# Performance work log

Hardware: AMD Instinct MI355X
Metric: run time of the kernel (lower is better)

Reference implementation:

```python
import jax, jax.numpy as jnp
import numpy as np

T, N, C, D, S = 512, 32, 1296, 512, 30
NORM_SCALE = 32.0
NEGINF = -1e9


def setup_inputs() -> dict:
    key = jax.random.key(0)
    k1, k2, k3, k4, k5 = jax.random.split(key, 5)
    feats = jax.random.normal(k1, (T * N, D), dtype=jnp.float32)
    classifier_weight = jax.random.normal(k2, (D, C), dtype=jnp.float32)
    labeling = jax.random.randint(k3, (N, S), 1, C)  # targets cannot be blank(0)
    logit_lgts = (T - jax.random.randint(k4, (N,), 0, 32)).astype(jnp.int32)
    labeling_lgts = (S - jax.random.randint(k5, (N,), 0, 5)).astype(jnp.int32)
    return dict(feats=feats, classifier_weight=classifier_weight,
                labeling=labeling, logit_lgts=logit_lgts, labeling_lgts=labeling_lgts)


def _ctc_loss(log_probs, labels, in_lens, lab_lens):
    # log_probs: (T, N, C); labels: (N, S); blank = 0; reduction = 'sum'
    Tt, Nn, Cc = log_probs.shape
    Ss = labels.shape[1]
    L = 2 * Ss + 1
    # extended labeling: blank, l1, blank, l2, ..., blank  -> (N, L)
    ext = jnp.zeros((Nn, L), dtype=labels.dtype).at[:, 1::2].set(labels)
    # gather per-state log-probs: (T, N, L)
    lp_ext = jnp.take_along_axis(log_probs, jnp.broadcast_to(ext[None], (Tt, Nn, L)), axis=2)
    # skip transition s-2 -> s allowed iff s > 1 and ext[s] != ext[s-2]
    skip_ok = jnp.concatenate(
        [jnp.zeros((Nn, 2), dtype=bool), ext[:, 2:] != ext[:, :-2]], axis=1)
    alpha0 = (jnp.full((Nn, L), NEGINF, dtype=log_probs.dtype)
              .at[:, 0].set(lp_ext[0, :, 0])
              .at[:, 1].set(lp_ext[0, :, 1]))

    def step(alpha, inp):
        lp_t, t = inp  # lp_t: (N, L)
        a1 = alpha
        a2 = jnp.pad(alpha[:, :-1], ((0, 0), (1, 0)), constant_values=NEGINF)
        a3 = jnp.where(skip_ok,
                       jnp.pad(alpha[:, :-2], ((0, 0), (2, 0)), constant_values=NEGINF),
                       NEGINF)
        new = jax.nn.logsumexp(jnp.stack([a1, a2, a3], axis=0), axis=0) + lp_t
        # freeze alpha once t reaches a sample's input length
        alpha = jnp.where((t < in_lens)[:, None], new, alpha)
        return alpha, None

    alpha, _ = jax.lax.scan(step, alpha0, (lp_ext[1:], jnp.arange(1, Tt)))
    Ln = 2 * lab_lens + 1  # (N,)
    last = jnp.take_along_axis(alpha, (Ln - 1)[:, None], axis=1)[:, 0]
    last2 = jnp.take_along_axis(alpha, (Ln - 2)[:, None], axis=1)[:, 0]
    nll = -jnp.logaddexp(last, last2)
    return jnp.sum(nll)


def reference(feats, classifier_weight, labeling, logit_lgts, labeling_lgts):
    # RadialCTC: cosine logits with norm_scale, then CTC on log-softmax.
    w_n = classifier_weight / jnp.linalg.norm(classifier_weight, axis=0, keepdims=True)  # (D, C)
    f_n = feats / jnp.linalg.norm(feats, axis=1, keepdims=True)  # (T*N, D)
    logits = NORM_SCALE * (f_n @ w_n)  # (T*N, C)
    log_probs = jax.nn.log_softmax(logits.reshape(T, N, C), axis=-1)
    return _ctc_loss(log_probs, labeling, logit_lgts, labeling_lgts)
```

## Files before the change

kernel.cpp:

```cpp
#include <hip/hip_runtime.h>
#include <stdint.h>
#include <stddef.h>


typedef _Float16 f16;
typedef _Float16 f16x8 __attribute__((ext_vector_type(8)));
typedef float f32x4 __attribute__((ext_vector_type(4)));
typedef __attribute__((address_space(1))) void* as1_void_ptr;
typedef __attribute__((address_space(3))) void* as3_void_ptr;

#define TT 512
#define NN 32
#define CC 1296
#define DD 512
#define SS 30
#define CP 1408
#define LL 61
#define NEGINF (-1e9f)
#define NORM_SCALE 32.0f
#define LOG2E 1.4426950408889634f
#define LN2   0.6931471805599453f

__device__ __forceinline__ float fexp2(float x) { return __builtin_amdgcn_exp2f(x); }
__device__ __forceinline__ float flog2(float x) { return __builtin_amdgcn_logf(x); }

__device__ __forceinline__ double dpp_sr1_zero64(double x) {
    long long b = __double_as_longlong(x);
    int lo = (int)(b & 0xFFFFFFFFLL);
    int hi = (int)(b >> 32);
    int lo2 = __builtin_amdgcn_update_dpp(0, lo, 0x138, 0xF, 0xF, false);
    int hi2 = __builtin_amdgcn_update_dpp(0, hi, 0x138, 0xF, 0xF, false);
    return __longlong_as_double(((long long)hi2 << 32) |
                                (unsigned long long)(unsigned int)lo2);
}
template <int CTRL>
__device__ __forceinline__ int dpp_imax_level(int m) {
    int t = __builtin_amdgcn_update_dpp(0, m, CTRL, 0xF, 0xF, false);
    return m > t ? m : t;
}

__global__ void colnorm_kernel(const float* __restrict__ W, float* __restrict__ ssq) {
    int c = blockIdx.x * 64 + threadIdx.x;
    if (c >= CC) return;
    int d0 = blockIdx.y * 64;
    float ss = 0.f;
    #pragma unroll 8
    for (int d = d0; d < d0 + 64; ++d) {
        float v = W[(size_t)d * CC + c];
        ss += v * v;
    }
    atomicAdd(&ssq[c], ss);
}

__global__ void wt_kernel(const float* __restrict__ W, const float* __restrict__ ssq,
                          f16* __restrict__ wt) {
    int idx = blockIdx.x * 256 + threadIdx.x;
    int c = idx >> 9, d = idx & 511;
    float v = 0.f;
    if (c < CC) v = W[(size_t)d * CC + c] * rsqrtf(ssq[c]);
    wt[idx] = (f16)v;
}

__global__ __launch_bounds__(256) void fnorm_kernel(const float* __restrict__ feats,
                                                    f16* __restrict__ fn) {
    int wv = (blockIdx.x * 256 + threadIdx.x) >> 6;
    int lane = threadIdx.x & 63;
    const float4* src = (const float4*)(feats + (size_t)wv * DD) + lane * 2;
    float4 a = src[0], b = src[1];
    float ss = a.x*a.x + a.y*a.y + a.z*a.z + a.w*a.w
             + b.x*b.x + b.y*b.y + b.z*b.z + b.w*b.w;
    #pragma unroll
    for (int off = 32; off; off >>= 1) ss += __shfl_xor(ss, off);
    float r = rsqrtf(ss);
    f16x8 o;
    o[0]=(f16)(a.x*r); o[1]=(f16)(a.y*r); o[2]=(f16)(a.z*r); o[3]=(f16)(a.w*r);
    o[4]=(f16)(b.x*r); o[5]=(f16)(b.y*r); o[6]=(f16)(b.z*r); o[7]=(f16)(b.w*r);
    *(f16x8*)(fn + (size_t)wv * DD + lane * 8) = o;
}

__global__ __launch_bounds__(256) void gemm_sumexp_kernel(const f16* __restrict__ A,
                                                          const f16* __restrict__ B,
                                                          float* __restrict__ sumexp) {
    __shared__ __align__(16) f16 As[128 * 32];
    __shared__ __align__(16) f16 Bs[128 * 32];
    int bm = blockIdx.x, bn = blockIdx.y;
    int tid = threadIdx.x;
    int w = tid >> 6, lane = tid & 63;
    int wm = w >> 1, wn = w & 1;
    int lm = lane & 15, hi = lane >> 4;
    int sw = (lm >> 1) & 3;
    f32x4 acc[4][4];
    f32x4 zero = {0.f, 0.f, 0.f, 0.f};
    #pragma unroll
    for (int i = 0; i < 4; ++i)
        #pragma unroll
        for (int j = 0; j < 4; ++j) acc[i][j] = zero;

    for (int kb = 0; kb < 16; ++kb) {
        #pragma unroll
        for (int p = 0; p < 2; ++p) {
            int s = p * 256 + tid;
            int row = s >> 2;
            int ch = (s & 3) ^ ((row >> 1) & 3);
            const f16* ga = A + (size_t)(bm * 128 + row) * DD + kb * 32 + ch * 8;
            const f16* gb = B + (size_t)(bn * 128 + row) * DD + kb * 32 + ch * 8;
            __builtin_amdgcn_global_load_lds((as1_void_ptr)ga,
                (as3_void_ptr)&As[(p * 256 + w * 64) * 8], 16, 0, 0);
            __builtin_amdgcn_global_load_lds((as1_void_ptr)gb,
                (as3_void_ptr)&Bs[(p * 256 + w * 64) * 8], 16, 0, 0);
        }
        __syncthreads();
        f16x8 af[4], bf[4];
        #pragma unroll
        for (int i = 0; i < 4; ++i)
            af[i] = *(const f16x8*)&As[(wm * 64 + i * 16 + lm) * 32 + (hi ^ sw) * 8];
        #pragma unroll
        for (int j = 0; j < 4; ++j)
            bf[j] = *(const f16x8*)&Bs[(wn * 64 + j * 16 + lm) * 32 + (hi ^ sw) * 8];
        #pragma unroll
        for (int i = 0; i < 4; ++i)
            #pragma unroll
            for (int j = 0; j < 4; ++j)
                acc[i][j] = __builtin_amdgcn_mfma_f32_16x16x32_f16(af[i], bf[j], acc[i][j], 0, 0, 0);
        __syncthreads();
    }
    #pragma unroll
    for (int i = 0; i < 4; ++i) {
        float rs[4] = {0.f, 0.f, 0.f, 0.f};
        #pragma unroll
        for (int j = 0; j < 4; ++j) {
            int c = bn * 128 + wn * 64 + j * 16 + lm;
            bool ok = (c < CC);
            #pragma unroll
            for (int r = 0; r < 4; ++r)
                rs[r] += ok ? fexp2(acc[i][j][r] * (NORM_SCALE * LOG2E)) : 0.f;
        }
        #pragma unroll
        for (int off = 1; off < 16; off <<= 1) {
            #pragma unroll
            for (int r = 0; r < 4; ++r) rs[r] += __shfl_xor(rs[r], off);
        }
        if (lm == 0) {
            int rowb = bm * 128 + wm * 64 + i * 16 + hi * 4;
            #pragma unroll
            for (int r = 0; r < 4; ++r) atomicAdd(&sumexp[rowb + r], rs[r]);
        }
    }
}

__global__ __launch_bounds__(256) void gather_kernel(const f16* __restrict__ fn,
                                                     const f16* __restrict__ wt,
                                                     const float* __restrict__ sumexp,
                                                     const int* __restrict__ labels,
                                                     float* __restrict__ lp_lab) {
    __shared__ __align__(16) f16 Bs[16 * 32 * 32];
    __shared__ __align__(16) f16 As[16 * 64 * 32];
    __shared__ float ls2[64];
    int n = blockIdx.x, t0 = blockIdx.y * 64;
    int tid = threadIdx.x;
    int w = tid >> 6, lane = tid & 63;
    int lm = lane & 15, hi = lane >> 4;
    int sw = (lm >> 1) & 3;

    #pragma unroll
    for (int it = 0; it < 8; ++it) {
        int s = it * 256 + tid;
        int row = (s >> 2) & 31;
        int ch = (s & 3) ^ ((row >> 1) & 3);
        int cls = (row == 0 || row > SS) ? 0 : labels[n * SS + row - 1];
        const f16* gb = wt + (size_t)cls * DD + (s >> 7) * 32 + ch * 8;
        __builtin_amdgcn_global_load_lds((as1_void_ptr)gb,
            (as3_void_ptr)&Bs[(it * 256 + w * 64) * 8], 16, 0, 0);
    }
    #pragma unroll
    for (int it = 0; it < 16; ++it) {
        int s = it * 256 + tid;
        int kb = s >> 8, row = (s >> 2) & 63;
        int ch = (s & 3) ^ ((row >> 1) & 3);
        const f16* ga = fn + (size_t)((t0 + row) * NN + n) * DD + kb * 32 + ch * 8;
        __builtin_amdgcn_global_load_lds((as1_void_ptr)ga,
            (as3_void_ptr)&As[(it * 256 + w * 64) * 8], 16, 0, 0);
    }
    if (tid < 64) ls2[tid] = flog2(sumexp[(size_t)(t0 + tid) * NN + n]);
    __syncthreads();

    f32x4 acc[2];
    acc[0] = (f32x4){0.f, 0.f, 0.f, 0.f};
    acc[1] = (f32x4){0.f, 0.f, 0.f, 0.f};
    #pragma unroll
    for (int kb = 0; kb < 16; ++kb) {
        f16x8 af  = *(const f16x8*)&As[kb * 2048 + (w * 16 + lm) * 32 + (hi ^ sw) * 8];
        f16x8 bf0 = *(const f16x8*)&Bs[kb * 1024 + lm * 32 + (hi ^ sw) * 8];
        f16x8 bf1 = *(const f16x8*)&Bs[kb * 1024 + (16 + lm) * 32 + (hi ^ sw) * 8];
        acc[0] = __builtin_amdgcn_mfma_f32_16x16x32_f16(af, bf0, acc[0], 0, 0, 0);
        acc[1] = __builtin_amdgcn_mfma_f32_16x16x32_f16(af, bf1, acc[1], 0, 0, 0);
    }
    #pragma unroll
    for (int jn = 0; jn < 2; ++jn) {
        int j = jn * 16 + lm;
        if (j >= 31) continue;
        float* dst = lp_lab + ((size_t)n * 31 + j) * TT + t0;
        #pragma unroll
        for (int r = 0; r < 4; ++r) {
            int tl = w * 16 + hi * 4 + r;
            dst[tl] = acc[jn][r] * (NORM_SCALE * LOG2E) - ls2[tl];
        }
    }
}

__global__ void ctc_kernel(const float* __restrict__ lp_lab, const int* __restrict__ labels,
                           const int* __restrict__ in_lens, const int* __restrict__ lab_lens,
                           float* __restrict__ nll) {
    int n = blockIdx.x;
    int s = threadIdx.x;
    bool valid = s < LL;
    int ext = (valid && (s & 1)) ? labels[n * SS + (s >> 1)] : 0;
    int jmap = (valid && (s & 1)) ? ((s >> 1) + 1) : 0;
    int ext2 = __shfl_up(ext, 2);
    double skipd = ((s >= 2) && valid && (ext != ext2)) ? 1.0 : 0.0;
    int Tin = in_lens[n];
    const float4* g0 = (const float4*)(lp_lab + ((size_t)n * 31 + jmap) * TT);

    float4 cur = g0[0];
    float4 nxt = g0[1];
    float4 nx2 = g0[2];
    double beta = (s <= 1) ? (double)fexp2(cur.x) : 0.0;
    int Mi = 0;

    auto stepL = [&](float lp) {
        double P = (double)fexp2(lp);
        double b1 = dpp_sr1_zero64(beta);
        double b2 = dpp_sr1_zero64(b1);
        beta = (beta + b1 + b2 * skipd) * P;
    };
    auto renorm = [&]() {
        int h = (int)(__double_as_longlong(beta) >> 32);
        h = dpp_imax_level<0x111>(h);
        h = dpp_imax_level<0x112>(h);
        h = dpp_imax_level<0x114>(h);
        h = dpp_imax_level<0x118>(h);
        int r0 = __builtin_amdgcn_readlane(h, 15);
        int r1 = __builtin_amdgcn_readlane(h, 31);
        int r2 = __builtin_amdgcn_readlane(h, 47);
        int r3 = __builtin_amdgcn_readlane(h, 63);
        int mx = max(max(r0, r1), max(r2, r3));
        int e11 = mx >> 20;
        double scale = __longlong_as_double((long long)(2046 - e11) << 52);
        beta *= scale;
        Mi += e11 - 1023;
    };

    stepL(cur.y); stepL(cur.z); stepL(cur.w);
    renorm();
    int remaining = Tin - 4;
    int g = 1;
    while (remaining >= 4) {
        cur = nxt; nxt = nx2;
        int gi = g + 2; if (gi > 127) gi = 127;
        nx2 = g0[gi];
        stepL(cur.x); stepL(cur.y); stepL(cur.z); stepL(cur.w);
        renorm();
        remaining -= 4; ++g;
    }
    cur = nxt;
    if (remaining > 0) stepL(cur.x);
    if (remaining > 1) stepL(cur.y);
    if (remaining > 2) stepL(cur.z);

    int Ln = 2 * lab_lens[n] + 1;
    double last  = __shfl(beta, Ln - 1);
    double last2 = __shfl(beta, Ln - 2);
    double sm = last + last2;
    long long bb = __double_as_longlong(sm);
    int e = (int)(bb >> 52) - 1023;
    double mant = __longlong_as_double((bb & 0xFFFFFFFFFFFFFLL) | (1023LL << 52));
    float v = -(flog2((float)mant) + (float)(e + Mi)) * LN2;
    if (s == 0) nll[n] = v;
}

__global__ void reduce_kernel(const float* __restrict__ nll, float* __restrict__ out) {
    int s = threadIdx.x;
    float v = (s < NN) ? nll[s] : 0.f;
    #pragma unroll
    for (int off = 32; off; off >>= 1) v += __shfl_xor(v, off);
    if (s == 0) out[0] = v;
}

extern "C" void kernel_launch(void* const* d_in, const int* in_sizes, int n_in,
                              void* d_out, int out_size, void* d_ws, size_t ws_size,
                              hipStream_t stream) {
    const float* feats        = (const float*)d_in[0];
    const float* W            = (const float*)d_in[1];
    const int*   labeling     = (const int*)d_in[2];
    const int*   logit_lgts   = (const int*)d_in[3];
    const int*   labeling_lgts= (const int*)d_in[4];
    float* out = (float*)d_out;
    char* ws = (char*)d_ws;

    size_t off = 0;
    f16*   wt     = (f16*)(ws + off);   off += (size_t)CP * DD * 2;
    f16*   fn     = (f16*)(ws + off);   off += (size_t)TT * NN * DD * 2;
    float* ssq    = (float*)(ws + off); off += 1312 * 4;
    float* sumexp = (float*)(ws + off); off += (size_t)TT * NN * 4;
    float* lp_lab = (float*)(ws + off); off += (size_t)NN * 31 * TT * 4;
    float* nllb   = (float*)(ws + off); off += 64 * 4;

    hipMemsetAsync(ssq, 0, 1312 * 4, stream);
    hipMemsetAsync(sumexp, 0, (size_t)TT * NN * 4, stream);

    colnorm_kernel<<<dim3((CC + 63) / 64, 8), 64, 0, stream>>>(W, ssq);
    wt_kernel<<<(CP * DD) / 256, 256, 0, stream>>>(W, ssq, wt);
    fnorm_kernel<<<(TT * NN) / 4, 256, 0, stream>>>(feats, fn);
    gemm_sumexp_kernel<<<dim3(TT * NN / 128, CP / 128), 256, 0, stream>>>(fn, wt, sumexp);
    gather_kernel<<<dim3(NN, TT / 64), 256, 0, stream>>>(fn, wt, sumexp, labeling, lp_lab);
    ctc_kernel<<<NN, 64, 0, stream>>>(lp_lab, labeling, logit_lgts, labeling_lgts, nllb);
    reduce_kernel<<<1, 64, 0, stream>>>(nllb, out);

    (void)in_sizes; (void)n_in; (void)out_size; (void)ws_size;
}
```

Before: 163.3 us.

## Fuse prep kernels and memsets into one launch, fold final reduction into CTC

Replaces colnorm, wt, fnorm kernels and two memsets with a single prep kernel whose blocks are partitioned by role: weight column normalization with shared-memory reduction, zeroing sumexp and a counter, and feature normalization. The final sum over samples moves into the CTC kernel via an atomic counter with last-block-done reduction. This removes several launches and their serialization gaps. In exchange the weight-column blocks read W with strided column access, and the reduction relies on threadfence/atomic ordering.

Measured after the change: 162.9 us. About the same (-0.3%).

```diff
diff --git a/kernel.cpp b/kernel.cpp
--- a/kernel.cpp
+++ b/kernel.cpp
@@ -21,6 +21,10 @@
 #define LOG2E 1.4426950408889634f
 #define LN2   0.6931471805599453f
 
+#define PREP_WBLK (CP / 16)
+#define PREP_ZBLK 17
+#define PREP_FBLK (TT * NN / 4)
+
 __device__ __forceinline__ float fexp2(float x) { return __builtin_amdgcn_exp2f(x); }
 __device__ __forceinline__ float flog2(float x) { return __builtin_amdgcn_logf(x); }
 
@@ -39,43 +43,68 @@
     return m > t ? m : t;
 }
 
-__global__ void colnorm_kernel(const float* __restrict__ W, float* __restrict__ ssq) {
-    int c = blockIdx.x * 64 + threadIdx.x;
-    if (c >= CC) return;
-    int d0 = blockIdx.y * 64;
-    float ss = 0.f;
-    #pragma unroll 8
-    for (int d = d0; d < d0 + 64; ++d) {
-        float v = W[(size_t)d * CC + c];
-        ss += v * v;
-    }
-    atomicAdd(&ssq[c], ss);
-}
-
-__global__ void wt_kernel(const float* __restrict__ W, const float* __restrict__ ssq,
-                          f16* __restrict__ wt) {
-    int idx = blockIdx.x * 256 + threadIdx.x;
-    int c = idx >> 9, d = idx & 511;
-    float v = 0.f;
-    if (c < CC) v = W[(size_t)d * CC + c] * rsqrtf(ssq[c]);
-    wt[idx] = (f16)v;
-}
-
-__global__ __launch_bounds__(256) void fnorm_kernel(const float* __restrict__ feats,
-                                                    f16* __restrict__ fn) {
-    int wv = (blockIdx.x * 256 + threadIdx.x) >> 6;
-    int lane = threadIdx.x & 63;
-    const float4* src = (const float4*)(feats + (size_t)wv * DD) + lane * 2;
-    float4 a = src[0], b = src[1];
-    float ss = a.x*a.x + a.y*a.y + a.z*a.z + a.w*a.w
-             + b.x*b.x + b.y*b.y + b.z*b.z + b.w*b.w;
-    #pragma unroll
-    for (int off = 32; off; off >>= 1) ss += __shfl_xor(ss, off);
-    float r = rsqrtf(ss);
-    f16x8 o;
-    o[0]=(f16)(a.x*r); o[1]=(f16)(a.y*r); o[2]=(f16)(a.z*r); o[3]=(f16)(a.w*r);
-    o[4]=(f16)(b.x*r); o[5]=(f16)(b.y*r); o[6]=(f16)(b.z*r); o[7]=(f16)(b.w*r);
-    *(f16x8*)(fn + (size_t)wv * DD + lane * 8) = o;
+__global__ __launch_bounds__(256) void prep_kernel(const float* __restrict__ W,
+                                                   const float* __restrict__ feats,
+                                                   f16* __restrict__ wt,
+                                                   f16* __restrict__ fn,
+                                                   float* __restrict__ sumexp,
+                                                   unsigned* __restrict__ ctr) {
+    int bx = blockIdx.x, tid = threadIdx.x;
+    if (bx < PREP_WBLK) {
+        __shared__ float red[256];
+        __shared__ float rqs[16];
+        int c0 = bx * 16;
+        int cl = tid & 15, dg = tid >> 4;
+        int c = c0 + cl;
+        float ss = 0.f;
+        if (c < CC) {
+            for (int d = dg; d < DD; d += 16) {
+                float v = W[(size_t)d * CC + c];
+                ss += v * v;
+            }
+        }
+        red[tid] = ss;
+        __syncthreads();
+        if (tid < 16) {
+            float s2 = 0.f;
+            #pragma unroll
+            for (int k = 0; k < 16; ++k) s2 += red[tid + 16 * k];
+            rqs[tid] = rsqrtf(s2);
+        }
+        __syncthreads();
+        int c_loc = tid >> 4, dl = tid & 15;
+        int cc = c0 + c_loc;
+        float rq = rqs[c_loc];
+        #pragma unroll 4
+        for (int it = 0; it < 32; ++it) {
+            int d = dl + it * 16;
+            float v = (cc < CC) ? W[(size_t)d * CC + cc] * rq : 0.f;
+            wt[(size_t)cc * DD + d] = (f16)v;
+        }
+    } else if (bx < PREP_WBLK + PREP_ZBLK) {
+        int zb = bx - PREP_WBLK;
+        if (zb < 16) {
+            float4 z = {0.f, 0.f, 0.f, 0.f};
+            ((float4*)sumexp)[zb * 256 + tid] = z;
+        } else if (tid == 0) {
+            *ctr = 0u;
+        }
+    } else {
+        int fb = bx - PREP_WBLK - PREP_ZBLK;
+        int wv = (fb * 256 + tid) >> 6;
+        int lane = tid & 63;
+        const float4* src = (const float4*)(feats + (size_t)wv * DD) + lane * 2;
+        float4 a = src[0], b = src[1];
+        float ss = a.x*a.x + a.y*a.y + a.z*a.z + a.w*a.w
+                 + b.x*b.x + b.y*b.y + b.z*b.z + b.w*b.w;
+        #pragma unroll
+        for (int off = 32; off; off >>= 1) ss += __shfl_xor(ss, off);
+        float r = rsqrtf(ss);
+        f16x8 o;
+        o[0]=(f16)(a.x*r); o[1]=(f16)(a.y*r); o[2]=(f16)(a.z*r); o[3]=(f16)(a.w*r);
+        o[4]=(f16)(b.x*r); o[5]=(f16)(b.y*r); o[6]=(f16)(b.z*r); o[7]=(f16)(b.w*r);
+        *(f16x8*)(fn + (size_t)wv * DD + lane * 8) = o;
+    }
 }
 
 __global__ __launch_bounds__(256) void gemm_sumexp_kernel(const f16* __restrict__ A,
@@ -210,7 +239,8 @@
 
 __global__ void ctc_kernel(const float* __restrict__ lp_lab, const int* __restrict__ labels,
                            const int* __restrict__ in_lens, const int* __restrict__ lab_lens,
-                           float* __restrict__ nll) {
+                           float* __restrict__ nll, unsigned* __restrict__ ctr,
+                           float* __restrict__ out) {
     int n = blockIdx.x;
     int s = threadIdx.x;
     bool valid = s < LL;
@@ -275,15 +305,17 @@
     int e = (int)(bb >> 52) - 1023;
     double mant = __longlong_as_double((bb & 0xFFFFFFFFFFFFFLL) | (1023LL << 52));
     float v = -(flog2((float)mant) + (float)(e + Mi)) * LN2;
-    if (s == 0) nll[n] = v;
-}
-
-__global__ void reduce_kernel(const float* __restrict__ nll, float* __restrict__ out) {
-    int s = threadIdx.x;
-    float v = (s < NN) ? nll[s] : 0.f;
-    #pragma unroll
-    for (int off = 32; off; off >>= 1) v += __shfl_xor(v, off);
-    if (s == 0) out[0] = v;
+    if (s == 0) {
+        nll[n] = v;
+        __threadfence();
+        unsigned old = atomicAdd(ctr, 1u);
+        if (old == NN - 1) {
+            __threadfence();
+            float t = 0.f;
+            for (int i = 0; i < NN; ++i) t += nll[i];
+            out[0] = t;
+        }
+    }
 }
 
 extern "C" void kernel_launch(void* const* d_in, const int* in_sizes, int n_in,
@@ -300,21 +332,17 @@
     size_t off = 0;
     f16*   wt     = (f16*)(ws + off);   off += (size_t)CP * DD * 2;
     f16*   fn     = (f16*)(ws + off);   off += (size_t)TT * NN * DD * 2;
-    float* ssq    = (float*)(ws + off); off += 1312 * 4;
     float* sumexp = (float*)(ws + off); off += (size_t)TT * NN * 4;
     float* lp_lab = (float*)(ws + off); off += (size_t)NN * 31 * TT * 4;
     float* nllb   = (float*)(ws + off); off += 64 * 4;
-
-    hipMemsetAsync(ssq, 0, 1312 * 4, stream);
-    hipMemsetAsync(sumexp, 0, (size_t)TT * NN * 4, stream);
-
-    colnorm_kernel<<<dim3((CC + 63) / 64, 8), 64, 0, stream>>>(W, ssq);
-    wt_kernel<<<(CP * DD) / 256, 256, 0, stream>>>(W, ssq, wt);
-    fnorm_kernel<<<(TT * NN) / 4, 256, 0, stream>>>(feats, fn);
+    unsigned* ctr = (unsigned*)(ws + off); off += 64;
+
+    prep_kernel<<<PREP_WBLK + PREP_ZBLK + PREP_FBLK, 256, 0, stream>>>(
+        W, feats, wt, fn, sumexp, ctr);
     gemm_sumexp_kernel<<<dim3(TT * NN / 128, CP / 128), 256, 0, stream>>>(fn, wt, sumexp);
     gather_kernel<<<dim3(NN, TT / 64), 256, 0, stream>>>(fn, wt, sumexp, labeling, lp_lab);
-    ctc_kernel<<<NN, 64, 0, stream>>>(lp_lab, labeling, logit_lgts, labeling_lgts, nllb);
-    reduce_kernel<<<1, 64, 0, stream>>>(nllb, out);
+    ctc_kernel<<<NN, 64, 0, stream>>>(lp_lab, labeling, logit_lgts, labeling_lgts,
+                                      nllb, ctr, out);
 
     (void)in_sizes; (void)n_in; (void)out_size; (void)ws_size;
 }
```
